# Performance work log

Hardware: AMD Instinct MI355X
Metric: run time of the kernel (lower is better)

Reference implementation:

```python
import jax, jax.numpy as jnp
import numpy as np

BN_EPS = 1e-5


def setup_inputs() -> dict:
    key = jax.random.key(0)
    k1, k2 = jax.random.split(key, 2)
    N_out, K, Cin, Cout = 65536, 8, 256, 512
    N_in = N_out * K
    data = jax.random.normal(k1, (N_in, Cin), dtype=jnp.float32)
    # Kaiming-ish scale for the conv weight [K*Cin, Cout]
    weight = jax.random.normal(k2, (K * Cin, Cout), dtype=jnp.float32) * (1.0 / np.sqrt(K * Cin))
    bias = jnp.zeros((Cout,), dtype=jnp.float32)
    gamma = jnp.ones((Cout,), dtype=jnp.float32)
    beta = jnp.zeros((Cout,), dtype=jnp.float32)
    # Full-octree stride-2 child indices: output node i gathers children 8i..8i+7
    neigh = jnp.arange(N_in, dtype=jnp.int64).reshape(N_out, K)
    return {"data": data, "weight": weight, "bias": bias,
            "gamma": gamma, "beta": beta, "neigh": neigh}


def reference(data, weight, bias, gamma, beta, neigh):
    # OctreeConv (kernel 2x2x2, stride 2, nempty): gather 8 children per output
    # node, then a single GEMM with weight [8*Cin, Cout].
    N_out, K = neigh.shape
    Cin = data.shape[1]
    feat = data[neigh.reshape(-1)].reshape(N_out, K * Cin)  # [N_out, 8*Cin]
    out = feat @ weight + bias                              # [N_out, Cout]
    # BatchNorm1d, training mode: biased batch stats over the node dim.
    mean = jnp.mean(out, axis=0)
    var = jnp.mean(jnp.square(out), axis=0) - jnp.square(mean)
    out = (out - mean) * jax.lax.rsqrt(var + BN_EPS) * gamma + beta
    return out
```

## Files before the change

kernel.cpp:

```cpp
#include <hip/hip_runtime.h>
#include <hip/hip_bf16.h>

typedef __attribute__((ext_vector_type(8))) short bf16x8;
typedef __attribute__((ext_vector_type(4))) float f32x4;

#define N_OUT 65536
#define CIN   256
#define COUT  512
#define BM    128
#define BN    256
#define BK    32
#define NKS   64

__device__ __forceinline__ unsigned short f2bf(float f) {
  union { __hip_bfloat16 h; unsigned short u; } c;
  c.h = __float2bfloat16(f);
  return c.u;
}

__device__ __forceinline__ float bf2f(unsigned short u) {
  union { unsigned int i; float f; } c;
  c.i = ((unsigned int)u) << 16;
  return c.f;
}

__device__ __forceinline__ bf16x8 pack8(f32x4 a, f32x4 b) {
  unsigned short u[8];
  u[0] = f2bf(a.x); u[1] = f2bf(a.y); u[2] = f2bf(a.z); u[3] = f2bf(a.w);
  u[4] = f2bf(b.x); u[5] = f2bf(b.y); u[6] = f2bf(b.z); u[7] = f2bf(b.w);
  return *reinterpret_cast<bf16x8*>(u);
}

__device__ __forceinline__ void gload_lds16u(const unsigned short* g, unsigned short* l) {
  __builtin_amdgcn_global_load_lds(
      (const __attribute__((address_space(1))) void*)g,
      (__attribute__((address_space(3))) void*)l, 16, 0, 0);
}

__global__ void wprep_kernel(const float* __restrict__ W, unsigned short* __restrict__ Wt) {
  int idx = blockIdx.x * blockDim.x + threadIdx.x;
  if (idx >= 64 * 4 * COUT) return;
  int n  = idx & (COUT - 1);
  int s  = (idx >> 9) & 3;
  int kb = idx >> 11;
  unsigned short tmp[8];
#pragma unroll
  for (int w = 0; w < 8; ++w)
    tmp[w] = f2bf(W[(size_t)(kb * 32 + s * 8 + w) * COUT + n]);
  *reinterpret_cast<bf16x8*>(Wt + ((size_t)kb * 16384 + s * 4096 + n * 8)) =
      *reinterpret_cast<bf16x8*>(tmp);
}

__global__ __launch_bounds__(512, 4) void gemm_kernel(
    const float* __restrict__ data,
    const int*   __restrict__ neigh,
    const unsigned short* __restrict__ Wt,
    float* __restrict__ out,
    unsigned short* __restrict__ raw,
    float* __restrict__ psum,
    float* __restrict__ psq)
{
  __shared__ union {
    struct {
      unsigned short a[3][BM * BK];
      unsigned short b[3][BK * BN];
    } r;
    struct { float S[2][BN]; float Q[2][BN]; } st;
  } sm;
  __shared__ unsigned int offs[BM * 8];

  const int tid = threadIdx.x;
  const int l   = tid & 63;
  const int w   = tid >> 6;
  const int wr  = w >> 2;
  const int wc  = w & 3;
  const int lg  = l >> 4;
  const int lm  = l & 15;

  const int bid = blockIdx.x;
  const int xcd = bid & 7;
  const int j   = bid >> 3;
  const int mb  = xcd * 64 + (j >> 1);
  const int nh  = j & 1;
  const int n0  = nh * BN;
  const int m0  = mb * BM;
  const int pidx = mb * 2 + nh;

  for (int e = tid; e < BM * 8; e += 512)
    offs[e] = ((unsigned)neigh[(size_t)m0 * 8 + e]) << 8;
  __syncthreads();

  f32x4 acc[4][4];
#pragma unroll
  for (int i = 0; i < 4; ++i)
#pragma unroll
    for (int jj = 0; jj < 4; ++jj) acc[i][jj] = (f32x4){0.f, 0.f, 0.f, 0.f};

  const int arow8 = (tid >> 2) * 8;
  const int achk8 = (tid & 3) * 8;
  const int awoff = (tid >> 2) * BK +
                    (((tid & 3) ^ ((tid >> 2) & 3) ^ ((tid >> 4) & 3)) << 3);
  const int aroff = (lg ^ (lm & 3) ^ ((lm >> 2) & 3)) << 3;

  const int q0 = w * 2;
  const unsigned short* bbase =
      Wt + n0 * 8 + (q0 >> 2) * 4096 + (q0 & 3) * 512 + l * 8;

  unsigned short *aA = sm.r.a[0], *aB = sm.r.a[1], *aC = sm.r.a[2];
  unsigned short *bA = sm.r.b[0], *bB = sm.r.b[1], *bC = sm.r.b[2];

  f32x4 X0, X1, Y0, Y1;

#define AG(T_, S0_, S1_) do { \
    int cn_ = (T_) >> 3, k0_ = ((T_) & 7) * BK; \
    const f32x4* p_ = reinterpret_cast<const f32x4*>(data + offs[arow8 + cn_] + k0_ + achk8); \
    S0_ = p_[0]; S1_ = p_[1]; \
  } while (0)

#define BD(T_, dst_) do { \
    const unsigned short* bs_ = bbase + (size_t)(T_) * 16384; \
    gload_lds16u(bs_,       (dst_) + q0 * 512); \
    gload_lds16u(bs_ + 512, (dst_) + q0 * 512 + 512); \
  } while (0)

#define COMPUTE(aP_, bP_) do { \
    bf16x8 af_[4]; \
    _Pragma("unroll") \
    for (int mi_ = 0; mi_ < 4; ++mi_) \
      af_[mi_] = *reinterpret_cast<const bf16x8*>( \
          (aP_) + (wr * 64 + mi_ * 16 + lm) * BK + aroff); \
    _Pragma("unroll") \
    for (int ni_ = 0; ni_ < 4; ++ni_) { \
      bf16x8 bb_ = *reinterpret_cast<const bf16x8*>( \
          (bP_) + lg * 2048 + (wc * 64 + ni_ * 16 + lm) * 8); \
      _Pragma("unroll") \
      for (int mi_ = 0; mi_ < 4; ++mi_) \
        acc[mi_][ni_] = __builtin_amdgcn_mfma_f32_16x16x32_bf16(af_[mi_], bb_, acc[mi_][ni_], 0, 0, 0); \
    } \
  } while (0)

#define BODY(t_, S0_, S1_) do { \
    if ((t_) <= NKS - 3)      asm volatile("s_waitcnt vmcnt(4)" ::: "memory"); \
    else if ((t_) == NKS - 2) asm volatile("s_waitcnt vmcnt(2)" ::: "memory"); \
    else                      asm volatile("s_waitcnt vmcnt(0)" ::: "memory"); \
    asm volatile("s_waitcnt lgkmcnt(0)" ::: "memory"); \
    __builtin_amdgcn_s_barrier(); \
    asm volatile("" ::: "memory"); \
    if ((t_) <= NKS - 3) { \
      *reinterpret_cast<bf16x8*>(aC + awoff) = pack8(S0_, S1_);   \
      BD((t_) + 2, bC); \
    } \
    if ((t_) <= NKS - 5) AG((t_) + 4, S0_, S1_); \
    COMPUTE(aA, bA); \
    asm volatile("" ::: "memory"); \
    { unsigned short* t0_ = aA; aA = aB; aB = aC; aC = t0_; } \
    { unsigned short* t1_ = bA; bA = bB; bB = bC; bC = t1_; } \
  } while (0)

  AG(0, X0, X1);
  AG(1, Y0, Y1);
  asm volatile("s_waitcnt vmcnt(2)" ::: "memory");
  *reinterpret_cast<bf16x8*>(sm.r.a[0] + awoff) = pack8(X0, X1);
  AG(2, X0, X1);
  BD(0, sm.r.b[0]);
  asm volatile("s_waitcnt vmcnt(4)" ::: "memory");
  *reinterpret_cast<bf16x8*>(sm.r.a[1] + awoff) = pack8(Y0, Y1);
  AG(3, Y0, Y1);
  BD(1, sm.r.b[1]);

#pragma unroll 1
  for (int t = 0; t < NKS; t += 2) {
    BODY(t,     X0, X1);
    BODY(t + 1, Y0, Y1);
  }

  if (raw) {
#pragma unroll
    for (int mi = 0; mi < 4; ++mi) {
#pragma unroll
      for (int r = 0; r < 4; ++r) {
        size_t row = (size_t)(m0 + wr * 64 + mi * 16 + lg * 4 + r);
        unsigned short* rp = raw + row * COUT + n0 + wc * 64 + lm;
#pragma unroll
        for (int ni = 0; ni < 4; ++ni) rp[ni * 16] = f2bf(acc[mi][ni][r]);
      }
    }
  } else {
#pragma unroll
    for (int mi = 0; mi < 4; ++mi) {
#pragma unroll
      for (int r = 0; r < 4; ++r) {
        size_t row = (size_t)(m0 + wr * 64 + mi * 16 + lg * 4 + r);
        float* op = out + row * COUT + n0 + wc * 64 + lm;
#pragma unroll
        for (int ni = 0; ni < 4; ++ni) op[ni * 16] = acc[mi][ni][r];
      }
    }
  }

  __syncthreads();
#pragma unroll
  for (int ni = 0; ni < 4; ++ni) {
    float s1 = 0.f, s2 = 0.f;
#pragma unroll
    for (int mi = 0; mi < 4; ++mi)
#pragma unroll
      for (int r = 0; r < 4; ++r) { float v = acc[mi][ni][r]; s1 += v; s2 += v * v; }
    s1 += __shfl_xor(s1, 16, 64); s1 += __shfl_xor(s1, 32, 64);
    s2 += __shfl_xor(s2, 16, 64); s2 += __shfl_xor(s2, 32, 64);
    if (l < 16) {
      sm.st.S[wr][wc * 64 + ni * 16 + l] = s1;
      sm.st.Q[wr][wc * 64 + ni * 16 + l] = s2;
    }
  }
  __syncthreads();
  if (tid < BN) {
    psum[(size_t)pidx * BN + tid] = sm.st.S[0][tid] + sm.st.S[1][tid];
  } else {
    int c = tid - BN;
    psq[(size_t)pidx * BN + c] = sm.st.Q[0][c] + sm.st.Q[1][c];
  }
#undef AG
#undef BD
#undef COMPUTE
#undef BODY
}

__global__ void reduce1_kernel(const float* __restrict__ psum, const float* __restrict__ psq,
                               float* __restrict__ p2) {
  int c = threadIdx.x, b = blockIdx.x;
  int h = c >> 8, crel = c & 255;
  float s = 0.f, q = 0.f;
#pragma unroll
  for (int jj = 0; jj < 8; ++jj) {
    size_t pi = (size_t)((b * 8 + jj) * 2 + h);
    s += psum[pi * 256 + crel];
    q += psq [pi * 256 + crel];
  }
  p2[b * 1024 + c] = s;
  p2[b * 1024 + 512 + c] = q;
}

__global__ void reduce2_kernel(const float* __restrict__ p2,
                               const float* __restrict__ gamma,
                               const float* __restrict__ beta,
                               float* __restrict__ scsh) {
  int c = threadIdx.x;
  float s = 0.f, q = 0.f;
  for (int b = 0; b < 64; ++b) { s += p2[b * 1024 + c]; q += p2[b * 1024 + 512 + c]; }
  float mean = s * (1.f / 65536.f);
  float var  = q * (1.f / 65536.f) - mean * mean;
  float rs   = rsqrtf(var + 1e-5f);
  float sc   = gamma[c] * rs;
  scsh[c] = sc;
  scsh[COUT + c] = beta[c] - mean * sc;
}

__global__ void bn_bf16_kernel(const unsigned short* __restrict__ raw,
                               float* __restrict__ out,
                               const float* __restrict__ scsh) {
  __shared__ float sc[COUT], sh[COUT];
  int t = threadIdx.x;
  sc[t] = scsh[t];
  sh[t] = scsh[COUT + t];
  __syncthreads();
  const bf16x8* r8 = reinterpret_cast<const bf16x8*>(raw);
  const size_t total  = (size_t)N_OUT * COUT / 8;
  const size_t stride = (size_t)gridDim.x * blockDim.x;
  for (size_t i = (size_t)blockIdx.x * blockDim.x + t; i < total; i += stride) {
    bf16x8 v = r8[i];
    int c0 = ((int)(i & 63)) * 8;
    f32x4 o0, o1;
    o0.x = bf2f((unsigned short)v[0]) * sc[c0]     + sh[c0];
    o0.y = bf2f((unsigned short)v[1]) * sc[c0 + 1] + sh[c0 + 1];
    o0.z = bf2f((unsigned short)v[2]) * sc[c0 + 2] + sh[c0 + 2];
    o0.w = bf2f((unsigned short)v[3]) * sc[c0 + 3] + sh[c0 + 3];
    o1.x = bf2f((unsigned short)v[4]) * sc[c0 + 4] + sh[c0 + 4];
    o1.y = bf2f((unsigned short)v[5]) * sc[c0 + 5] + sh[c0 + 5];
    o1.z = bf2f((unsigned short)v[6]) * sc[c0 + 6] + sh[c0 + 6];
    o1.w = bf2f((unsigned short)v[7]) * sc[c0 + 7] + sh[c0 + 7];
    f32x4* op = reinterpret_cast<f32x4*>(out + i * 8);
    op[0] = o0;
    op[1] = o1;
  }
}

__global__ void bn_kernel(float* __restrict__ out, const float* __restrict__ scsh) {
  __shared__ float sc[COUT], sh[COUT];
  int t = threadIdx.x;
  sc[t] = scsh[t];
  sh[t] = scsh[COUT + t];
  __syncthreads();
  f32x4* o4 = reinterpret_cast<f32x4*>(out);
  const size_t total  = (size_t)N_OUT * COUT / 4;
  const size_t stride = (size_t)gridDim.x * blockDim.x;
  for (size_t i = (size_t)blockIdx.x * blockDim.x + t; i < total; i += stride) {
    f32x4 v = o4[i];
    int c = ((int)(i & 127)) * 4;
    v.x = v.x * sc[c]     + sh[c];
    v.y = v.y * sc[c + 1] + sh[c + 1];
    v.z = v.z * sc[c + 2] + sh[c + 2];
    v.w = v.w * sc[c + 3] + sh[c + 3];
    o4[i] = v;
  }
}

extern "C" void kernel_launch(void* const* d_in, const int* in_sizes, int n_in,
                              void* d_out, int out_size, void* d_ws, size_t ws_size,
                              hipStream_t stream) {
  const float* data   = (const float*)d_in[0];
  const float* weight = (const float*)d_in[1];
  const float* gamma  = (const float*)d_in[3];
  const float* beta   = (const float*)d_in[4];
  const int*   neigh  = (const int*)d_in[5];
  float* out = (float*)d_out;

  char* ws = (char*)d_ws;
  unsigned short* Wt = (unsigned short*)ws;
  float* psum = (float*)(ws + (2u << 20));
  float* psq  = (float*)(ws + (3u << 20));
  float* p2   = (float*)(ws + (4u << 20));
  float* scsh = (float*)(ws + (4u << 20) + (256u << 10));

  const bool big = ws_size >= (72ull << 20);
  unsigned short* raw = big ? (unsigned short*)(ws + (8ull << 20)) : nullptr;

  wprep_kernel<<<512, 256, 0, stream>>>(weight, Wt);
  gemm_kernel<<<1024, 512, 0, stream>>>(data, neigh, Wt, out, raw, psum, psq);
  reduce1_kernel<<<64, 512, 0, stream>>>(psum, psq, p2);
  reduce2_kernel<<<1, 512, 0, stream>>>(p2, gamma, beta, scsh);
  if (big) bn_bf16_kernel<<<2048, 512, 0, stream>>>(raw, out, scsh);
  else     bn_kernel<<<2048, 512, 0, stream>>>(out, scsh);
}
```

Measured before the change: 258.7 us.

## Load gathered A fragments directly into registers, dropping the A LDS staging

Each wave now gathers its own A operand rows straight from global memory into registers in MFMA fragment layout and packs them to bf16 in place. This removes the A tile from shared memory along with its write, swizzle and read-back. Only the B tiles stay triple-buffered in LDS. The cost is redundant A loads across the four column-waves, more registers for deeper register prefetch, and launch bounds relaxed from 4 to 2 blocks per CU, so occupancy may fall.

```diff
diff --git a/kernel.cpp b/kernel.cpp
--- a/kernel.cpp
+++ b/kernel.cpp
@@ -51,7 +51,7 @@
       *reinterpret_cast<bf16x8*>(tmp);
 }
 
-__global__ __launch_bounds__(512, 4) void gemm_kernel(
+__global__ __launch_bounds__(512, 2) void gemm_kernel(
     const float* __restrict__ data,
     const int*   __restrict__ neigh,
     const unsigned short* __restrict__ Wt,
@@ -61,10 +61,7 @@
     float* __restrict__ psq)
 {
   __shared__ union {
-    struct {
-      unsigned short a[3][BM * BK];
-      unsigned short b[3][BK * BN];
-    } r;
+    unsigned short b[3][BK * BN];
     struct { float S[2][BN]; float Q[2][BN]; } st;
   } sm;
   __shared__ unsigned int offs[BM * 8];
@@ -96,25 +93,28 @@
 #pragma unroll
     for (int jj = 0; jj < 4; ++jj) acc[i][jj] = (f32x4){0.f, 0.f, 0.f, 0.f};
 
-  const int arow8 = (tid >> 2) * 8;
-  const int achk8 = (tid & 3) * 8;
-  const int awoff = (tid >> 2) * BK +
-                    (((tid & 3) ^ ((tid >> 2) & 3) ^ ((tid >> 4) & 3)) << 3);
-  const int aroff = (lg ^ (lm & 3) ^ ((lm >> 2) & 3)) << 3;
+  const int r0 = (wr * 64 + lm) * 8;
+  unsigned o0, o1, o2, o3;
+  unsigned p0, p1, p2, p3;
 
   const int q0 = w * 2;
   const unsigned short* bbase =
       Wt + n0 * 8 + (q0 >> 2) * 4096 + (q0 & 3) * 512 + l * 8;
 
-  unsigned short *aA = sm.r.a[0], *aB = sm.r.a[1], *aC = sm.r.a[2];
-  unsigned short *bA = sm.r.b[0], *bB = sm.r.b[1], *bC = sm.r.b[2];
-
-  f32x4 X0, X1, Y0, Y1;
-
-#define AG(T_, S0_, S1_) do { \
-    int cn_ = (T_) >> 3, k0_ = ((T_) & 7) * BK; \
-    const f32x4* p_ = reinterpret_cast<const f32x4*>(data + offs[arow8 + cn_] + k0_ + achk8); \
-    S0_ = p_[0]; S1_ = p_[1]; \
+  unsigned short *bA = sm.b[0], *bB = sm.b[1], *bC = sm.b[2];
+
+  f32x4 XA[8], YA[8];
+  bf16x8 af[4];
+
+#define AGS(j_, Q0_, Q1_, Q2_, Q3_, A_) do { \
+    const f32x4* a0_ = reinterpret_cast<const f32x4*>(data + (Q0_) + (j_) * 32 + lg * 8); \
+    const f32x4* a1_ = reinterpret_cast<const f32x4*>(data + (Q1_) + (j_) * 32 + lg * 8); \
+    const f32x4* a2_ = reinterpret_cast<const f32x4*>(data + (Q2_) + (j_) * 32 + lg * 8); \
+    const f32x4* a3_ = reinterpret_cast<const f32x4*>(data + (Q3_) + (j_) * 32 + lg * 8); \
+    A_[0] = a0_[0]; A_[1] = a0_[1]; \
+    A_[2] = a1_[0]; A_[3] = a1_[1]; \
+    A_[4] = a2_[0]; A_[5] = a2_[1]; \
+    A_[6] = a3_[0]; A_[7] = a3_[1]; \
   } while (0)
 
 #define BD(T_, dst_) do { \
@@ -123,55 +123,64 @@
     gload_lds16u(bs_ + 512, (dst_) + q0 * 512 + 512); \
   } while (0)
 
-#define COMPUTE(aP_, bP_) do { \
-    bf16x8 af_[4]; \
-    _Pragma("unroll") \
-    for (int mi_ = 0; mi_ < 4; ++mi_) \
-      af_[mi_] = *reinterpret_cast<const bf16x8*>( \
-          (aP_) + (wr * 64 + mi_ * 16 + lm) * BK + aroff); \
+#define PACK(A_) do { \
+    af[0] = pack8(A_[0], A_[1]); \
+    af[1] = pack8(A_[2], A_[3]); \
+    af[2] = pack8(A_[4], A_[5]); \
+    af[3] = pack8(A_[6], A_[7]); \
+  } while (0)
+
+#define MM(bP_) do { \
     _Pragma("unroll") \
     for (int ni_ = 0; ni_ < 4; ++ni_) { \
       bf16x8 bb_ = *reinterpret_cast<const bf16x8*>( \
           (bP_) + lg * 2048 + (wc * 64 + ni_ * 16 + lm) * 8); \
       _Pragma("unroll") \
       for (int mi_ = 0; mi_ < 4; ++mi_) \
-        acc[mi_][ni_] = __builtin_amdgcn_mfma_f32_16x16x32_bf16(af_[mi_], bb_, acc[mi_][ni_], 0, 0, 0); \
+        acc[mi_][ni_] = __builtin_amdgcn_mfma_f32_16x16x32_bf16(af[mi_], bb_, acc[mi_][ni_], 0, 0, 0); \
     } \
   } while (0)
 
-#define BODY(t_, S0_, S1_) do { \
-    if ((t_) <= NKS - 3)      asm volatile("s_waitcnt vmcnt(4)" ::: "memory"); \
-    else if ((t_) == NKS - 2) asm volatile("s_waitcnt vmcnt(2)" ::: "memory"); \
-    else                      asm volatile("s_waitcnt vmcnt(0)" ::: "memory"); \
+#define BODY(cn_, j_) do { \
+    if ((cn_) == 7 && (j_) == 7) asm volatile("s_waitcnt vmcnt(0)" ::: "memory"); \
+    else                         asm volatile("s_waitcnt vmcnt(18)" ::: "memory"); \
     asm volatile("s_waitcnt lgkmcnt(0)" ::: "memory"); \
     __builtin_amdgcn_s_barrier(); \
     asm volatile("" ::: "memory"); \
-    if ((t_) <= NKS - 3) { \
-      *reinterpret_cast<bf16x8*>(aC + awoff) = pack8(S0_, S1_);   \
-      BD((t_) + 2, bC); \
+    if (!((cn_) == 7 && (j_) >= 6)) BD((cn_) * 8 + (j_) + 2, bC); \
+    if ((j_) & 1) PACK(YA); else PACK(XA); \
+    if ((j_) <= 5) { \
+      if ((j_) & 1) AGS((j_) + 2, o0, o1, o2, o3, YA); \
+      else          AGS((j_) + 2, o0, o1, o2, o3, XA); \
+    } else if ((cn_) < 7) { \
+      if ((j_) == 6) AGS(0, p0, p1, p2, p3, XA); \
+      else           AGS(1, p0, p1, p2, p3, YA); \
     } \
-    if ((t_) <= NKS - 5) AG((t_) + 4, S0_, S1_); \
-    COMPUTE(aA, bA); \
+    MM(bA); \
     asm volatile("" ::: "memory"); \
-    { unsigned short* t0_ = aA; aA = aB; aB = aC; aC = t0_; } \
-    { unsigned short* t1_ = bA; bA = bB; bB = bC; bC = t1_; } \
-  } while (0)
-
-  AG(0, X0, X1);
-  AG(1, Y0, Y1);
-  asm volatile("s_waitcnt vmcnt(2)" ::: "memory");
-  *reinterpret_cast<bf16x8*>(sm.r.a[0] + awoff) = pack8(X0, X1);
-  AG(2, X0, X1);
-  BD(0, sm.r.b[0]);
-  asm volatile("s_waitcnt vmcnt(4)" ::: "memory");
-  *reinterpret_cast<bf16x8*>(sm.r.a[1] + awoff) = pack8(Y0, Y1);
-  AG(3, Y0, Y1);
-  BD(1, sm.r.b[1]);
+    { unsigned short* t_ = bA; bA = bB; bB = bC; bC = t_; } \
+  } while (0)
+
+  o0 = offs[r0];
+  o1 = offs[r0 + 128];
+  o2 = offs[r0 + 256];
+  o3 = offs[r0 + 384];
+  AGS(0, o0, o1, o2, o3, XA);
+  BD(0, sm.b[0]);
+  AGS(1, o0, o1, o2, o3, YA);
+  BD(1, sm.b[1]);
 
 #pragma unroll 1
-  for (int t = 0; t < NKS; t += 2) {
-    BODY(t,     X0, X1);
-    BODY(t + 1, Y0, Y1);
+  for (int cn = 0; cn < 8; ++cn) {
+    if (cn < 7) {
+      p0 = offs[r0 + cn + 1];
+      p1 = offs[r0 + 128 + cn + 1];
+      p2 = offs[r0 + 256 + cn + 1];
+      p3 = offs[r0 + 384 + cn + 1];
+    }
+    BODY(cn, 0); BODY(cn, 1); BODY(cn, 2); BODY(cn, 3);
+    BODY(cn, 4); BODY(cn, 5); BODY(cn, 6); BODY(cn, 7);
+    o0 = p0; o1 = p1; o2 = p2; o3 = p3;
   }
 
   if (raw) {
@@ -220,9 +229,10 @@
     int c = tid - BN;
     psq[(size_t)pidx * BN + c] = sm.st.Q[0][c] + sm.st.Q[1][c];
   }
-#undef AG
+#undef AGS
 #undef BD
-#undef COMPUTE
+#undef PACK
+#undef MM
 #undef BODY
 }
 
```

Result: slower. 637.3 us (+146.4%).
